# Kernel optimization log

Hardware: AMD Instinct MI355X
Metric: run time of the kernel (lower is better)

Reference implementation:

```python
import jax, jax.numpy as jnp
import numpy as np


def _bs_matrix(n):
    # Kronecker product of n copies of the 2x2 beam-splitter unitary.
    bs = (1.0 / np.sqrt(2.0)) * np.array([[1 + 0j, 0 + 1j], [0 + 1j, 1 + 0j]], dtype=np.complex128)
    M = np.array([[1.0 + 0j]], dtype=np.complex128)
    for _ in range(n):
        M = np.kron(M, bs)
    return jnp.asarray(M, dtype=jnp.complex64)  # [2^n, 2^n]


def _phase_shifts(phi0, phi1, n):
    # Equivalent to phase_shifts_to_tensor_product_space_v2:
    # phi[i] = sum_q (phi1[q] if bit_{n-1-q}(i) else phi0[q]); returns exp(i*phi).
    N = 2 ** n
    bits = (jnp.arange(N)[:, None] >> (n - 1 - jnp.arange(n))[None, :]) & 1  # [N, n]
    bits = bits.astype(phi0.dtype)
    phi = jnp.sum(bits * phi1 + (1.0 - bits) * phi0, axis=-1)  # [N]
    return jax.lax.complex(jnp.cos(phi), jnp.sin(phi))


def setup_inputs() -> dict:
    n = 12
    N = 2 ** n
    B = 2048
    key = jax.random.key(0)
    kx, ka, kb, kt, kp = jax.random.split(key, 5)
    TWO_PI = 2.0 * np.pi
    return {
        "x": jax.random.normal(kx, (B, 2, N), dtype=jnp.float32),
        "alphas": jax.random.uniform(ka, (n,), dtype=jnp.float32, minval=0.0, maxval=TWO_PI),
        "betas": jax.random.uniform(kb, (n,), dtype=jnp.float32, minval=0.0, maxval=TWO_PI),
        "thetas": jax.random.uniform(kt, (n,), dtype=jnp.float32, minval=0.0, maxval=TWO_PI),
        "phis": jax.random.uniform(kp, (n,), dtype=jnp.float32, minval=0.0, maxval=TWO_PI),
    }


def reference(x, alphas, betas, thetas, phis):
    n = alphas.shape[0]
    bs = _bs_matrix(n)  # [N, N] complex
    input_shifts = _phase_shifts(alphas, betas, n)                       # [N]
    theta_shifts = _phase_shifts(thetas, jnp.zeros_like(thetas), n)      # [N]
    phi_shifts = _phase_shifts(phis, jnp.zeros_like(phis), n)            # [N]

    z = jax.lax.complex(x[:, 0, :], x[:, 1, :])  # [B, N]
    out = (input_shifts * z) @ bs
    out = (theta_shifts * out) @ bs
    out = phi_shifts * out
    return jnp.stack([jnp.real(out), jnp.imag(out)], axis=1)  # [B, 2, N]
```

## Files before the change

### kernel.cpp

```cpp
#include <hip/hip_runtime.h>
#include <math.h>

#define NQ 12
#define NN 4096

typedef float f2 __attribute__((ext_vector_type(2)));

__device__ __forceinline__ float2 cmulh(float2 a, float2 b) {
    return make_float2(a.x * b.x - a.y * b.y, a.x * b.y + a.y * b.x);
}

__device__ __forceinline__ void cmac_pk(f2& acc, f2 m, f2 b) {
    asm("v_pk_fma_f32 %0, %1, %2, %0 op_sel:[0,0,0] op_sel_hi:[0,1,1]\n\t"
        "v_pk_fma_f32 %0, %1, %2, %0 op_sel:[1,1,0] op_sel_hi:[1,0,1] neg_lo:[1,0,0]"
        : "+v"(acc) : "s"(m), "v"(b));
}
__device__ __forceinline__ void cmul_pk(f2& r, f2 m, f2 b) {
    asm("v_pk_mul_f32 %0, %1, %2 op_sel:[0,0] op_sel_hi:[0,1]\n\t"
        "v_pk_fma_f32 %0, %1, %2, %0 op_sel:[1,1,0] op_sel_hi:[1,0,1] neg_lo:[1,0,0]"
        : "=&v"(r) : "s"(m), "v"(b));
}

template<int D>
__device__ __forceinline__ void stagepk(f2 (&v)[16], f2 m00, f2 m01, f2 m10, f2 m11) {
    #pragma unroll
    for (int s = 0; s < 16; ++s) {
        if (s & D) continue;
        f2 va = v[s], vb = v[s | D];
        f2 r0, r1;
        cmul_pk(r0, m00, va); cmac_pk(r0, m01, vb);
        cmul_pk(r1, m10, va); cmac_pk(r1, m11, vb);
        v[s] = r0; v[s | D] = r1;
    }
}

__global__ void setup_mats(const float* __restrict__ alphas,
                           const float* __restrict__ betas,
                           const float* __restrict__ thetas,
                           const float* __restrict__ phis,
                           float2* __restrict__ Mg) {
    int t = threadIdx.x;
    if (t < NQ) {
        int p = t, q = NQ - 1 - p;
        float sa, ca, sb, cb, st, ct, sf, cf;
        sincosf(alphas[q], &sa, &ca);
        sincosf(betas[q],  &sb, &cb);
        sincosf(thetas[q], &st, &ct);
        sincosf(phis[q],   &sf, &cf);
        float2 A  = make_float2(ca, sa);
        float2 Bb = make_float2(cb, sb);
        float2 F  = make_float2(cf, sf);
        float2 Tm  = make_float2(0.5f * (ct - 1.0f), 0.5f * st);
        float2 Tp  = make_float2(0.5f * (ct + 1.0f), 0.5f * st);
        float2 iTp = make_float2(-Tp.y, Tp.x);
        Mg[p * 4 + 0] = cmulh(cmulh(F, Tm), A);
        Mg[p * 4 + 1] = cmulh(cmulh(F, iTp), Bb);
        Mg[p * 4 + 2] = cmulh(iTp, A);
        Mg[p * 4 + 3] = cmulh(make_float2(-Tm.x, -Tm.y), Bb);
    }
}

__global__ __launch_bounds__(256) void sq_layer(const float* __restrict__ x,
                                                const float2* __restrict__ Mgf,
                                                float* __restrict__ out) {
    __shared__ f2 lds[NN];
    const int T = threadIdx.x;
    const size_t rowoff = (size_t)blockIdx.x * (2 * NN);
    const f2* Mg = (const f2*)Mgf;

    f2 v[16];
    #pragma unroll
    for (int rhi = 0; rhi < 4; ++rhi) {
        int base = (rhi << 10) + (T << 2);
        float4 re4 = *reinterpret_cast<const float4*>(x + rowoff + base);
        float4 im4 = *reinterpret_cast<const float4*>(x + rowoff + NN + base);
        v[rhi * 4 + 0] = f2{re4.x, im4.x};
        v[rhi * 4 + 1] = f2{re4.y, im4.y};
        v[rhi * 4 + 2] = f2{re4.z, im4.z};
        v[rhi * 4 + 3] = f2{re4.w, im4.w};
    }

    stagepk<1>(v, Mg[0],  Mg[1],  Mg[2],  Mg[3]);
    stagepk<2>(v, Mg[4],  Mg[5],  Mg[6],  Mg[7]);
    stagepk<4>(v, Mg[40], Mg[41], Mg[42], Mg[43]);
    stagepk<8>(v, Mg[44], Mg[45], Mg[46], Mg[47]);

    {
        const int baseA = (T << 2) ^ ((T >> 2) & 0xF);
        #pragma unroll
        for (int s = 0; s < 16; ++s)
            lds[((s >> 2) << 10) | (baseA ^ (s & 3))] = v[s];
    }
    __syncthreads();
    const int bB = ((T >> 6) << 10) | (((T >> 2) & 0xF) << 6) | (T & 3);
    const int cB = bB ^ ((((T >> 2) & 3)) << 2);
    #pragma unroll
    for (int s = 0; s < 16; ++s) v[s] = lds[cB ^ ((s << 2) ^ (s >> 2))];

    stagepk<1>(v, Mg[8],  Mg[9],  Mg[10], Mg[11]);
    stagepk<2>(v, Mg[12], Mg[13], Mg[14], Mg[15]);
    stagepk<4>(v, Mg[16], Mg[17], Mg[18], Mg[19]);
    stagepk<8>(v, Mg[20], Mg[21], Mg[22], Mg[23]);

    #pragma unroll
    for (int s = 0; s < 16; ++s) lds[cB ^ ((s << 2) ^ (s >> 2))] = v[s];
    const int bC = ((T >> 6) << 10) | (T & 63);
    const int cC = bC ^ ((T >> 4) & 3);
    #pragma unroll
    for (int s = 0; s < 16; ++s) v[s] = lds[(cC ^ ((s & 3) << 2)) | (s << 6)];

    stagepk<1>(v, Mg[24], Mg[25], Mg[26], Mg[27]);
    stagepk<2>(v, Mg[28], Mg[29], Mg[30], Mg[31]);
    stagepk<4>(v, Mg[32], Mg[33], Mg[34], Mg[35]);
    stagepk<8>(v, Mg[36], Mg[37], Mg[38], Mg[39]);

    #pragma unroll
    for (int s = 0; s < 16; ++s) {
        int i = bC | (s << 6);
        out[rowoff + i]      = v[s].x;
        out[rowoff + NN + i] = v[s].y;
    }
}

extern "C" void kernel_launch(void* const* d_in, const int* in_sizes, int n_in,
                              void* d_out, int out_size, void* d_ws, size_t ws_size,
                              hipStream_t stream) {
    const float* x      = (const float*)d_in[0];
    const float* alphas = (const float*)d_in[1];
    const float* betas  = (const float*)d_in[2];
    const float* thetas = (const float*)d_in[3];
    const float* phis   = (const float*)d_in[4];
    float* out = (float*)d_out;
    float2* Mg = (float2*)d_ws;

    const int B = in_sizes[0] / (2 * NN);

    hipLaunchKernelGGL(setup_mats, dim3(1), dim3(64), 0, stream,
                       alphas, betas, thetas, phis, Mg);
    hipLaunchKernelGGL(sq_layer, dim3(B), dim3(256), 0, stream,
                       x, (const float2*)Mg, out);
}
```

Baseline: 33.72 us.

## Split per-row transform across 512 threads with 8 elements and padded LDS

Each row's 12-qubit butterfly network is now handled by 512 threads holding 8 complex values each, instead of 256 threads holding 16. The transform becomes four rounds of three radix-2 stages with LDS transposes between them. A stride-9 padded shared-memory layout replaces the XOR swizzle, and the first two exchanges stay within a wavefront, so only one block barrier remains. The aim is lower register pressure, higher occupancy and fewer barriers, paid for with one extra LDS round trip and a larger shared buffer.

```diff
diff --git a/kernel.cpp b/kernel.cpp
--- a/kernel.cpp
+++ b/kernel.cpp
@@ -22,9 +22,9 @@
 }
 
 template<int D>
-__device__ __forceinline__ void stagepk(f2 (&v)[16], f2 m00, f2 m01, f2 m10, f2 m11) {
+__device__ __forceinline__ void stagepk8(f2 (&v)[8], f2 m00, f2 m01, f2 m10, f2 m11) {
     #pragma unroll
-    for (int s = 0; s < 16; ++s) {
+    for (int s = 0; s < 8; ++s) {
         if (s & D) continue;
         f2 va = v[s], vb = v[s | D];
         f2 r0, r1;
@@ -60,63 +60,80 @@
     }
 }
 
-__global__ __launch_bounds__(256) void sq_layer(const float* __restrict__ x,
-                                                const float2* __restrict__ Mgf,
-                                                float* __restrict__ out) {
-    __shared__ f2 lds[NN];
+__global__ __launch_bounds__(512, 8) void sq_layer(const float* __restrict__ x,
+                                                   const float2* __restrict__ Mgf,
+                                                   float* __restrict__ out) {
+    __shared__ f2 lds[4608];
     const int T = threadIdx.x;
     const size_t rowoff = (size_t)blockIdx.x * (2 * NN);
     const f2* Mg = (const f2*)Mgf;
 
-    f2 v[16];
-    #pragma unroll
-    for (int rhi = 0; rhi < 4; ++rhi) {
-        int base = (rhi << 10) + (T << 2);
-        float4 re4 = *reinterpret_cast<const float4*>(x + rowoff + base);
-        float4 im4 = *reinterpret_cast<const float4*>(x + rowoff + NN + base);
-        v[rhi * 4 + 0] = f2{re4.x, im4.x};
-        v[rhi * 4 + 1] = f2{re4.y, im4.y};
-        v[rhi * 4 + 2] = f2{re4.z, im4.z};
-        v[rhi * 4 + 3] = f2{re4.w, im4.w};
+    f2 v[8];
+    {
+        const float* px = x + rowoff + (T << 3);
+        float4 ra = *reinterpret_cast<const float4*>(px);
+        float4 rb = *reinterpret_cast<const float4*>(px + 4);
+        float4 ia = *reinterpret_cast<const float4*>(px + NN);
+        float4 ib = *reinterpret_cast<const float4*>(px + NN + 4);
+        v[0] = f2{ra.x, ia.x}; v[1] = f2{ra.y, ia.y};
+        v[2] = f2{ra.z, ia.z}; v[3] = f2{ra.w, ia.w};
+        v[4] = f2{rb.x, ib.x}; v[5] = f2{rb.y, ib.y};
+        v[6] = f2{rb.z, ib.z}; v[7] = f2{rb.w, ib.w};
     }
 
-    stagepk<1>(v, Mg[0],  Mg[1],  Mg[2],  Mg[3]);
-    stagepk<2>(v, Mg[4],  Mg[5],  Mg[6],  Mg[7]);
-    stagepk<4>(v, Mg[40], Mg[41], Mg[42], Mg[43]);
-    stagepk<8>(v, Mg[44], Mg[45], Mg[46], Mg[47]);
+    stagepk8<1>(v, Mg[0],  Mg[1],  Mg[2],  Mg[3]);
+    stagepk8<2>(v, Mg[4],  Mg[5],  Mg[6],  Mg[7]);
+    stagepk8<4>(v, Mg[8],  Mg[9],  Mg[10], Mg[11]);
 
     {
-        const int baseA = (T << 2) ^ ((T >> 2) & 0xF);
+        f2* wp = lds + 9 * T;
         #pragma unroll
-        for (int s = 0; s < 16; ++s)
-            lds[((s >> 2) << 10) | (baseA ^ (s & 3))] = v[s];
+        for (int s = 0; s < 8; ++s) wp[s] = v[s];
+    }
+    {
+        const f2* rp = lds + 72 * (T >> 3) + (T & 7);
+        #pragma unroll
+        for (int s = 0; s < 8; ++s) v[s] = rp[9 * s];
+    }
+
+    stagepk8<1>(v, Mg[12], Mg[13], Mg[14], Mg[15]);
+    stagepk8<2>(v, Mg[16], Mg[17], Mg[18], Mg[19]);
+    stagepk8<4>(v, Mg[20], Mg[21], Mg[22], Mg[23]);
+
+    {
+        f2* wp = lds + 72 * (T >> 3) + (T & 7);
+        #pragma unroll
+        for (int s = 0; s < 8; ++s) wp[9 * s] = v[s];
+    }
+    {
+        const f2* rp = lds + 576 * (T >> 6) + (T & 63) + ((T & 63) >> 3);
+        #pragma unroll
+        for (int s = 0; s < 8; ++s) v[s] = rp[72 * s];
+    }
+
+    stagepk8<1>(v, Mg[24], Mg[25], Mg[26], Mg[27]);
+    stagepk8<2>(v, Mg[28], Mg[29], Mg[30], Mg[31]);
+    stagepk8<4>(v, Mg[32], Mg[33], Mg[34], Mg[35]);
+
+    {
+        f2* wp = lds + 576 * (T >> 6) + (T & 63) + ((T & 63) >> 3);
+        #pragma unroll
+        for (int s = 0; s < 8; ++s) wp[72 * s] = v[s];
     }
     __syncthreads();
-    const int bB = ((T >> 6) << 10) | (((T >> 2) & 0xF) << 6) | (T & 3);
-    const int cB = bB ^ ((((T >> 2) & 3)) << 2);
-    #pragma unroll
-    for (int s = 0; s < 16; ++s) v[s] = lds[cB ^ ((s << 2) ^ (s >> 2))];
+    {
+        const f2* rp = lds + T + (T >> 3);
+        #pragma unroll
+        for (int s = 0; s < 8; ++s) v[s] = rp[576 * s];
+    }
 
-    stagepk<1>(v, Mg[8],  Mg[9],  Mg[10], Mg[11]);
-    stagepk<2>(v, Mg[12], Mg[13], Mg[14], Mg[15]);
-    stagepk<4>(v, Mg[16], Mg[17], Mg[18], Mg[19]);
-    stagepk<8>(v, Mg[20], Mg[21], Mg[22], Mg[23]);
+    stagepk8<1>(v, Mg[36], Mg[37], Mg[38], Mg[39]);
+    stagepk8<2>(v, Mg[40], Mg[41], Mg[42], Mg[43]);
+    stagepk8<4>(v, Mg[44], Mg[45], Mg[46], Mg[47]);
 
     #pragma unroll
-    for (int s = 0; s < 16; ++s) lds[cB ^ ((s << 2) ^ (s >> 2))] = v[s];
-    const int bC = ((T >> 6) << 10) | (T & 63);
-    const int cC = bC ^ ((T >> 4) & 3);
-    #pragma unroll
-    for (int s = 0; s < 16; ++s) v[s] = lds[(cC ^ ((s & 3) << 2)) | (s << 6)];
-
-    stagepk<1>(v, Mg[24], Mg[25], Mg[26], Mg[27]);
-    stagepk<2>(v, Mg[28], Mg[29], Mg[30], Mg[31]);
-    stagepk<4>(v, Mg[32], Mg[33], Mg[34], Mg[35]);
-    stagepk<8>(v, Mg[36], Mg[37], Mg[38], Mg[39]);
-
-    #pragma unroll
-    for (int s = 0; s < 16; ++s) {
-        int i = bC | (s << 6);
+    for (int s = 0; s < 8; ++s) {
+        int i = (s << 9) | T;
         out[rowoff + i]      = v[s].x;
         out[rowoff + NN + i] = v[s].y;
     }
@@ -137,6 +154,6 @@
 
     hipLaunchKernelGGL(setup_mats, dim3(1), dim3(64), 0, stream,
                        alphas, betas, thetas, phis, Mg);
-    hipLaunchKernelGGL(sq_layer, dim3(B), dim3(256), 0, stream,
+    hipLaunchKernelGGL(sq_layer, dim3(B), dim3(512), 0, stream,
                        x, (const float2*)Mg, out);
 }
```

Result: faster. 32.68 us (-3.1%).
